# Performance work log

Hardware: AMD Instinct MI355X
Metric: run time of the kernel (lower is better)

## Reference

```python
import jax, jax.numpy as jnp
import numpy as np

N = 10000          # nodes
E = 160000         # edges (avg degree 16)
IN_DIM = 10
OUT_DIM = 3
EDGE_DIM = 9
HIDDEN = 256
HEADS = 8
C = HIDDEN // HEADS  # 32 per-head channels
T = 5
BN_EPS = 1e-5
LRELU_SLOPE = 0.2  # GATv2Conv negative_slope default


def setup_inputs() -> dict:
    key = jax.random.key(0)
    ks = jax.random.split(key, 16)
    g = lambda k, shape, scale: jax.random.normal(k, shape, dtype=jnp.float32) * scale
    s = 1.0 / np.sqrt(HIDDEN)
    inp = {}
    inp['x'] = g(ks[0], (N, IN_DIM), 1.0)
    inp['edge_attr'] = g(ks[1], (E, EDGE_DIM), 1.0)
    inp['edge_index'] = jax.random.randint(ks[2], (2, E), 0, N, dtype=jnp.int32)
    # lift
    inp['lift_W'] = g(ks[3], (IN_DIM, HIDDEN), 1.0 / np.sqrt(IN_DIM))
    inp['lift_b'] = jnp.zeros((HIDDEN,), jnp.float32)
    # T stacked GATv2 layers
    inp['Wl'] = g(ks[4], (T, HIDDEN, HIDDEN), s)
    inp['bl'] = jnp.zeros((T, HIDDEN), jnp.float32)
    inp['Wr'] = g(ks[5], (T, HIDDEN, HIDDEN), s)
    inp['br'] = jnp.zeros((T, HIDDEN), jnp.float32)
    inp['We'] = g(ks[6], (T, EDGE_DIM, HIDDEN), 1.0 / np.sqrt(EDGE_DIM))
    inp['att'] = g(ks[7], (T, HEADS, C), 1.0 / np.sqrt(C))
    inp['conv_bias'] = jnp.zeros((T, HIDDEN), jnp.float32)
    inp['bn_gamma'] = jnp.ones((T, HIDDEN), jnp.float32)
    inp['bn_beta'] = jnp.zeros((T, HIDDEN), jnp.float32)
    # projection MLP: Lin-BN-ReLU, Lin-BN-ReLU, Lin
    inp['p1_W'] = g(ks[8], (HIDDEN, HIDDEN), s)
    inp['p1_b'] = jnp.zeros((HIDDEN,), jnp.float32)
    inp['pbn1_g'] = jnp.ones((HIDDEN,), jnp.float32)
    inp['pbn1_b'] = jnp.zeros((HIDDEN,), jnp.float32)
    inp['p2_W'] = g(ks[9], (HIDDEN, HIDDEN), s)
    inp['p2_b'] = jnp.zeros((HIDDEN,), jnp.float32)
    inp['pbn2_g'] = jnp.ones((HIDDEN,), jnp.float32)
    inp['pbn2_b'] = jnp.zeros((HIDDEN,), jnp.float32)
    inp['p3_W'] = g(ks[10], (HIDDEN, OUT_DIM), s)
    inp['p3_b'] = jnp.zeros((OUT_DIM,), jnp.float32)
    return inp


def _bn(h, gamma, beta):
    # BatchNorm1d with batch statistics (biased variance), eps=1e-5
    mu = h.mean(axis=0)
    var = jnp.var(h, axis=0)
    return gamma * (h - mu) * jax.lax.rsqrt(var + BN_EPS) + beta


def _forward(x, edge_attr, edge_index, lift_W, lift_b, Wl, bl, Wr, br, We, att,
             conv_bias, bn_gamma, bn_beta, p1_W, p1_b, pbn1_g, pbn1_b,
             p2_W, p2_b, pbn2_g, pbn2_b, p3_W, p3_b):
    src = edge_index[0]  # message source j
    dst = edge_index[1]  # message target i (softmax segments)
    # per_graph_edge_norm on cols 0:9 (== full edge_dim), single graph (batch=None):
    # per-column z-score over all edges of the graph
    ea = (edge_attr - edge_attr.mean(axis=0)) / (edge_attr.std(axis=0) + 1e-8)
    h = jax.nn.relu(x @ lift_W + lift_b)  # [N, HIDDEN]
    for t in range(T):
        xl = (h @ Wl[t] + bl[t]).reshape(N, HEADS, C)   # source transform
        xr = (h @ Wr[t] + br[t]).reshape(N, HEADS, C)   # target transform
        xe = (ea @ We[t]).reshape(E, HEADS, C)          # edge transform
        # GATv2: attention logits from leaky-relu'd summed features
        e = jax.nn.leaky_relu(xl[src] + xr[dst] + xe, LRELU_SLOPE)  # [E,H,C]
        logits = jnp.einsum('ehc,hc->eh', e, att[t])                # [E,H]
        # segment softmax over destination nodes
        m = jax.ops.segment_max(logits, dst, num_segments=N)
        m = jnp.where(jnp.isfinite(m), m, 0.0)
        z = jnp.exp(logits - m[dst])
        denom = jax.ops.segment_sum(z, dst, num_segments=N)
        alpha = z / (denom[dst] + 1e-16)                             # [E,H]
        agg = jax.ops.segment_sum(alpha[:, :, None] * xl[src], dst, num_segments=N)
        out = agg.reshape(N, HIDDEN) + conv_bias[t]
        h = jax.nn.elu(_bn(out, bn_gamma[t], bn_beta[t]))
    h = jax.nn.relu(_bn(h @ p1_W + p1_b, pbn1_g, pbn1_b))
    h = jax.nn.relu(_bn(h @ p2_W + p2_b, pbn2_g, pbn2_b))
    return h @ p3_W + p3_b  # [N, OUT_DIM]


def reference(x, edge_attr, edge_index, lift_W, lift_b, Wl, bl, Wr, br, We, att,
              conv_bias, bn_gamma, bn_beta, p1_W, p1_b, pbn1_g, pbn1_b,
              p2_W, p2_b, pbn2_g, pbn2_b, p3_W, p3_b):
    return _forward(x, edge_attr, edge_index, lift_W, lift_b, Wl, bl, Wr, br, We, att,
                    conv_bias, bn_gamma, bn_beta, p1_W, p1_b, pbn1_g, pbn1_b,
                    p2_W, p2_b, pbn2_g, pbn2_b, p3_W, p3_b)
```

## Files before the change

kernel.cpp:

```cpp
#include <hip/hip_runtime.h>

#define Nn 10000
#define Ee 160000
#define HID 256
#define EDIM 9
#define INDIM 10
#define Tt 5

typedef _Float16 f16;
typedef _Float16 f16x8 __attribute__((ext_vector_type(8)));
typedef _Float16 f16x4 __attribute__((ext_vector_type(4)));
typedef float f32x4 __attribute__((ext_vector_type(4)));

__global__ __launch_bounds__(256) void colstats_kernel(const float* __restrict__ in,
                                                       float* __restrict__ cs) {
  float s[9], s2[9];
#pragma unroll
  for (int k = 0; k < 9; ++k) { s[k] = 0.f; s2[k] = 0.f; }
  for (int i = blockIdx.x * blockDim.x + threadIdx.x; i < Ee; i += gridDim.x * blockDim.x) {
#pragma unroll
    for (int k = 0; k < 9; ++k) {
      float v = in[i * 9 + k];
      s[k] += v; s2[k] += v * v;
    }
  }
#pragma unroll
  for (int k = 0; k < 9; ++k) {
    for (int off = 1; off < 64; off <<= 1) {
      s[k] += __shfl_xor(s[k], off);
      s2[k] += __shfl_xor(s2[k], off);
    }
  }
  if ((threadIdx.x & 63) == 0) {
#pragma unroll
    for (int k = 0; k < 9; ++k) {
      atomicAdd(&cs[k], s[k]);
      atomicAdd(&cs[16 + k], s2[k]);
    }
  }
}

__global__ __launch_bounds__(256) void lift_kernel(const float* __restrict__ x,
                                                   const float* __restrict__ W,
                                                   const float* __restrict__ b,
                                                   f16* __restrict__ hq) {
  __shared__ float xs[INDIM];
  int n = blockIdx.x, ch = threadIdx.x;
  if (ch < INDIM) xs[ch] = x[n * INDIM + ch];
  __syncthreads();
  float s = b[ch];
#pragma unroll
  for (int k = 0; k < INDIM; ++k) s += xs[k] * W[k * 256 + ch];
  hq[n * 256 + ch] = (f16)fmaxf(s, 0.f);
}

__global__ __launch_bounds__(256) void degree_kernel(const int* __restrict__ dst,
                                                     int* __restrict__ deg) {
  int e = blockIdx.x * 256 + threadIdx.x;
  if (e < Ee) atomicAdd(&deg[dst[e]], 1);
}

__global__ __launch_bounds__(1024) void scan_kernel(const int* __restrict__ deg,
                                                    int* __restrict__ rowptr,
                                                    int* __restrict__ cursor) {
  __shared__ int part[1024];
  int tid = threadIdx.x;
  const int CH = (Nn + 1023) / 1024;
  int start = tid * CH;
  int s = 0;
  for (int i = 0; i < CH; ++i) { int idx = start + i; if (idx < Nn) s += deg[idx]; }
  part[tid] = s;
  __syncthreads();
  for (int off = 1; off < 1024; off <<= 1) {
    int v = part[tid];
    int w = (tid >= off) ? part[tid - off] : 0;
    __syncthreads();
    part[tid] = v + w;
    __syncthreads();
  }
  int run = part[tid] - s;
  for (int i = 0; i < CH; ++i) {
    int idx = start + i;
    if (idx < Nn) { rowptr[idx] = run; cursor[idx] = run; run += deg[idx]; }
  }
  if (tid == 0) rowptr[Nn] = Ee;
}

__global__ __launch_bounds__(256) void fill_kernel(const int* __restrict__ dst,
                                                   int* __restrict__ cursor,
                                                   int* __restrict__ perm) {
  int e = blockIdx.x * 256 + threadIdx.x;
  if (e < Ee) {
    int pos = atomicAdd(&cursor[dst[e]], 1);
    perm[pos] = e;
  }
}

__global__ __launch_bounds__(256) void eaperm_kernel(const float* __restrict__ edge_attr,
                                                     const float* __restrict__ cs,
                                                     const int* __restrict__ perm,
                                                     const int* __restrict__ srcIn,
                                                     int* __restrict__ srcp,
                                                     float* __restrict__ eap) {
  int idx = blockIdx.x * 256 + threadIdx.x;
  if (idx >= Ee) return;
  int e = perm[idx];
  srcp[idx] = srcIn[e];
  const float* a = edge_attr + e * 9;
  float o[12];
#pragma unroll
  for (int k = 0; k < 9; ++k) {
    float mu = cs[k] * (1.f / Ee);
    float var = fmaxf(cs[16 + k] * (1.f / Ee) - mu * mu, 0.f);
    o[k] = (a[k] - mu) / (sqrtf(var) + 1e-8f);
  }
  o[9] = o[10] = o[11] = 0.f;
  float4 v0 = {o[0], o[1], o[2], o[3]};
  float4 v1 = {o[4], o[5], o[6], o[7]};
  float4 v2 = {o[8], o[9], o[10], o[11]};
  *(float4*)(eap + (size_t)idx * 12 + 0) = v0;
  *(float4*)(eap + (size_t)idx * 12 + 4) = v1;
  *(float4*)(eap + (size_t)idx * 12 + 8) = v2;
}

__global__ __launch_bounds__(256) void convert_kernel(const float* __restrict__ Wl,
                                                      const float* __restrict__ Wr,
                                                      const float* __restrict__ p1,
                                                      const float* __restrict__ p2,
                                                      f16* __restrict__ wt) {
  int nrow = blockIdx.x, s = blockIdx.y, k = threadIdx.x;
  const float* srcp; int n = nrow; size_t dst;
  if (s < 5) {
    dst = (size_t)s * 131072 + (size_t)nrow * 256 + k;
    if (nrow < 256) srcp = Wl + s * 65536;
    else { srcp = Wr + s * 65536; n = nrow - 256; }
  } else {
    if (nrow >= 256) return;
    dst = 655360 + (size_t)(s - 5) * 65536 + (size_t)nrow * 256 + k;
    srcp = (s == 5) ? p1 : p2;
  }
  wt[dst] = (f16)srcp[k * 256 + n];
}

__global__ __launch_bounds__(256) void prep_bias_kernel(const float* __restrict__ bl,
                                                        const float* __restrict__ br,
                                                        float* __restrict__ bc) {
  int idx = blockIdx.x * 256 + threadIdx.x;
  if (idx >= 2560) return;
  int t = idx >> 9, c = idx & 511;
  bc[idx] = (c < 256) ? bl[t * 256 + c] : br[t * 256 + c - 256];
}

__global__ __launch_bounds__(256) void gemm16_kernel(const f16* __restrict__ A,
                                                     const f16* __restrict__ BT,
                                                     const float* __restrict__ bias,
                                                     const float* __restrict__ sums,
                                                     const float* __restrict__ gamma,
                                                     const float* __restrict__ beta,
                                                     int act,
                                                     f16* __restrict__ out,
                                                     int M, int OS) {
  __shared__ __align__(16) f16 As[64][264];
  __shared__ __align__(16) f16 Bs[64][264];
  const int tid = threadIdx.x;
  const int wave = tid >> 6, lane = tid & 63;
  const int l15 = lane & 15, quad = lane >> 4;
  const int m0 = blockIdx.y * 64, n0 = blockIdx.x * 64;
  const int wm = (wave >> 1) * 32, wn = (wave & 1) * 32;
  const int colbase = (tid & 31) * 8, rowbase = tid >> 5;
  float sA[8], tA[8];
  if (act >= 0) {
#pragma unroll
    for (int c4 = 0; c4 < 2; ++c4) {
      float4 su = *(const float4*)(sums + colbase + c4 * 4);
      float4 sq = *(const float4*)(sums + 256 + colbase + c4 * 4);
      float4 g4 = *(const float4*)(gamma + colbase + c4 * 4);
      float4 b4 = *(const float4*)(beta + colbase + c4 * 4);
      float su_[4] = {su.x, su.y, su.z, su.w};
      float sq_[4] = {sq.x, sq.y, sq.z, sq.w};
      float g_[4] = {g4.x, g4.y, g4.z, g4.w};
      float b_[4] = {b4.x, b4.y, b4.z, b4.w};
#pragma unroll
      for (int c = 0; c < 4; ++c) {
        float mu = su_[c] * (1.f / Nn);
        float var = fmaxf(sq_[c] * (1.f / Nn) - mu * mu, 0.f);
        float is = rsqrtf(var + 1e-5f) * g_[c];
        sA[c4 * 4 + c] = is;
        tA[c4 * 4 + c] = b_[c] - mu * is;
      }
    }
  }
#pragma unroll
  for (int i = 0; i < 8; ++i) {
    int row = rowbase + 8 * i;
    f16x8 av = {};
    int gm = m0 + row;
    if (gm < M) av = *(const f16x8*)(A + (size_t)gm * 256 + colbase);
    if (act >= 0) {
#pragma unroll
      for (int e = 0; e < 8; ++e) {
        float y = (float)av[e] * sA[e] + tA[e];
        if (act == 0) y = y > 0.f ? y : (__expf(y) - 1.f);
        else y = fmaxf(y, 0.f);
        av[e] = (f16)y;
      }
    }
    *(f16x8*)(&As[row][colbase]) = av;
    f16x8 bv = *(const f16x8*)(BT + (size_t)(n0 + row) * 256 + colbase);
    *(f16x8*)(&Bs[row][colbase]) = bv;
  }
  __syncthreads();
  f32x4 zero4 = {0.f, 0.f, 0.f, 0.f};
  f32x4 acc[2][2] = {{zero4, zero4}, {zero4, zero4}};
#pragma unroll
  for (int kk = 0; kk < 256; kk += 32) {
    f16x8 a0 = *(const f16x8*)(&As[wm + l15][kk + quad * 8]);
    f16x8 a1 = *(const f16x8*)(&As[wm + 16 + l15][kk + quad * 8]);
    f16x8 b0 = *(const f16x8*)(&Bs[wn + l15][kk + quad * 8]);
    f16x8 b1 = *(const f16x8*)(&Bs[wn + 16 + l15][kk + quad * 8]);
    acc[0][0] = __builtin_amdgcn_mfma_f32_16x16x32_f16(a0, b0, acc[0][0], 0, 0, 0);
    acc[0][1] = __builtin_amdgcn_mfma_f32_16x16x32_f16(a0, b1, acc[0][1], 0, 0, 0);
    acc[1][0] = __builtin_amdgcn_mfma_f32_16x16x32_f16(a1, b0, acc[1][0], 0, 0, 0);
    acc[1][1] = __builtin_amdgcn_mfma_f32_16x16x32_f16(a1, b1, acc[1][1], 0, 0, 0);
  }
  __syncthreads();
  f16* Cs = (f16*)&As[0][0];
#pragma unroll
  for (int ni = 0; ni < 2; ++ni) {
    int nl = wn + ni * 16 + l15;
    float bv = bias[n0 + nl];
#pragma unroll
    for (int mi = 0; mi < 2; ++mi)
#pragma unroll
      for (int r = 0; r < 4; ++r)
        Cs[(wm + mi * 16 + quad * 4 + r) * 72 + nl] = (f16)(acc[mi][ni][r] + bv);
  }
  __syncthreads();
  {
    int row = tid >> 2, c4 = (tid & 3) * 16;
    int gm = m0 + row;
    if (gm < M) {
      f16x8 v0 = *(const f16x8*)(&Cs[row * 72 + c4]);
      f16x8 v1 = *(const f16x8*)(&Cs[row * 72 + c4 + 8]);
      *(f16x8*)(out + (size_t)gm * OS + n0 + c4) = v0;
      *(f16x8*)(out + (size_t)gm * OS + n0 + c4 + 8) = v1;
    }
  }
}

__global__ __launch_bounds__(256) void gat_fused(const f16* __restrict__ hxlr,
                                                 const float* __restrict__ eap,
                                                 const int* __restrict__ srcp,
                                                 const int* __restrict__ rowptr,
                                                 const float* __restrict__ We_t,
                                                 const float* __restrict__ att_t,
                                                 const float* __restrict__ cb_t,
                                                 f16* __restrict__ outb) {
  int wave = threadIdx.x >> 6, lane = threadIdx.x & 63;
  int i = blockIdx.x * 4 + wave;
  if (i >= Nn) return;
  int ch = lane * 4;
  float we[9][4];
#pragma unroll
  for (int k = 0; k < 9; ++k) {
    float4 w4 = *(const float4*)(We_t + k * 256 + ch);
    we[k][0] = w4.x; we[k][1] = w4.y; we[k][2] = w4.z; we[k][3] = w4.w;
  }
  float4 a4 = *(const float4*)(att_t + ch);
  float att[4] = {a4.x, a4.y, a4.z, a4.w};
  f16x4 xr4 = *(const f16x4*)(hxlr + (size_t)i * 512 + 256 + ch);
  float xri[4] = {(float)xr4[0], (float)xr4[1], (float)xr4[2], (float)xr4[3]};
  float acc[4] = {0.f, 0.f, 0.f, 0.f};
  float d = 0.f;
  int r0 = rowptr[i], r1 = rowptr[i + 1];
  for (int base = r0; base < r1; base += 4) {
    int cnt = r1 - base;
    int ib[4];
#pragma unroll
    for (int b = 0; b < 4; ++b) ib[b] = base + (b < cnt ? b : cnt - 1);
    int js[4];
#pragma unroll
    for (int b = 0; b < 4; ++b) js[b] = srcp[ib[b]];
    float xlv[4][4];
#pragma unroll
    for (int b = 0; b < 4; ++b) {
      f16x4 v4 = *(const f16x4*)(hxlr + (size_t)js[b] * 512 + ch);
      xlv[b][0] = (float)v4[0]; xlv[b][1] = (float)v4[1];
      xlv[b][2] = (float)v4[2]; xlv[b][3] = (float)v4[3];
    }
    float sp[4];
#pragma unroll
    for (int b = 0; b < 4; ++b) {
      const float* ep = eap + (size_t)ib[b] * 12;
      float4 e0 = *(const float4*)ep;
      float4 e1 = *(const float4*)(ep + 4);
      float e8 = ep[8];
      float s = 0.f;
#pragma unroll
      for (int c = 0; c < 4; ++c) {
        float v = xlv[b][c] + xri[c];
        v += e0.x * we[0][c] + e0.y * we[1][c] + e0.z * we[2][c] + e0.w * we[3][c];
        v += e1.x * we[4][c] + e1.y * we[5][c] + e1.z * we[6][c] + e1.w * we[7][c];
        v += e8 * we[8][c];
        v = v > 0.f ? v : 0.2f * v;
        s += att[c] * v;
      }
      sp[b] = s;
    }
#pragma unroll
    for (int b = 0; b < 4; ++b) {
      sp[b] += __shfl_xor(sp[b], 1);
      sp[b] += __shfl_xor(sp[b], 2);
      sp[b] += __shfl_xor(sp[b], 4);
    }
#pragma unroll
    for (int b = 0; b < 4; ++b) {
      float z = (b < cnt) ? __expf(fminf(sp[b], 75.f)) : 0.f;
      d += z;
#pragma unroll
      for (int c = 0; c < 4; ++c) acc[c] += z * xlv[b][c];
    }
  }
  float inv = 1.f / (d + 1e-16f);
  float4 cb4 = *(const float4*)(cb_t + ch);
  f16x4 o;
  o[0] = (f16)(acc[0] * inv + cb4.x);
  o[1] = (f16)(acc[1] * inv + cb4.y);
  o[2] = (f16)(acc[2] * inv + cb4.z);
  o[3] = (f16)(acc[3] * inv + cb4.w);
  *(f16x4*)(outb + (size_t)i * 256 + ch) = o;
}

__global__ __launch_bounds__(256) void bn_stats_kernel(const f16* __restrict__ v,
                                                       float* __restrict__ sums) {
  __shared__ float ls[512];
  int tid = threadIdx.x;
  for (int i = tid; i < 512; i += 256) ls[i] = 0.f;
  __syncthreads();
  int wave = tid >> 6, lane = tid & 63, ch = lane * 4;
  float s[4] = {0.f, 0.f, 0.f, 0.f}, s2[4] = {0.f, 0.f, 0.f, 0.f};
  for (int r = blockIdx.x * 4 + wave; r < Nn; r += gridDim.x * 4) {
    f16x4 x4 = *(const f16x4*)(v + (size_t)r * 256 + ch);
#pragma unroll
    for (int c = 0; c < 4; ++c) {
      float x = (float)x4[c];
      s[c] += x; s2[c] += x * x;
    }
  }
#pragma unroll
  for (int c = 0; c < 4; ++c) {
    atomicAdd(&ls[ch + c], s[c]);
    atomicAdd(&ls[256 + ch + c], s2[c]);
  }
  __syncthreads();
  for (int i = tid; i < 512; i += 256) atomicAdd(&sums[i], ls[i]);
}

__global__ __launch_bounds__(256) void final_kernel(const f16* __restrict__ hq,
                                                    const float* __restrict__ sums,
                                                    const float* __restrict__ gamma,
                                                    const float* __restrict__ beta,
                                                    const float* __restrict__ W,
                                                    const float* __restrict__ b,
                                                    float* __restrict__ out3) {
  int wave = threadIdx.x >> 6, lane = threadIdx.x & 63;
  int n = blockIdx.x * 4 + wave;
  if (n >= Nn) return;
  int ch = lane * 4;
  float4 su = *(const float4*)(sums + ch);
  float4 sq = *(const float4*)(sums + 256 + ch);
  float4 g4 = *(const float4*)(gamma + ch);
  float4 b4 = *(const float4*)(beta + ch);
  float su_[4] = {su.x, su.y, su.z, su.w};
  float sq_[4] = {sq.x, sq.y, sq.z, sq.w};
  float g_[4] = {g4.x, g4.y, g4.z, g4.w};
  float bb_[4] = {b4.x, b4.y, b4.z, b4.w};
  f16x4 h4 = *(const f16x4*)(hq + (size_t)n * 256 + ch);
  float s0 = 0.f, s1 = 0.f, s2 = 0.f;
#pragma unroll
  for (int c = 0; c < 4; ++c) {
    float mu = su_[c] * (1.f / Nn);
    float var = fmaxf(sq_[c] * (1.f / Nn) - mu * mu, 0.f);
    float is = rsqrtf(var + 1e-5f) * g_[c];
    float y = fmaxf(((float)h4[c] - mu) * is + bb_[c], 0.f);
    const float* w = W + (ch + c) * 3;
    s0 += y * w[0]; s1 += y * w[1]; s2 += y * w[2];
  }
  for (int off = 1; off < 64; off <<= 1) {
    s0 += __shfl_xor(s0, off);
    s1 += __shfl_xor(s1, off);
    s2 += __shfl_xor(s2, off);
  }
  if (lane == 0) {
    out3[n * 3 + 0] = s0 + b[0];
    out3[n * 3 + 1] = s1 + b[1];
    out3[n * 3 + 2] = s2 + b[2];
  }
}

extern "C" void kernel_launch(void* const* d_in, const int* in_sizes, int n_in,
                              void* d_out, int out_size, void* d_ws, size_t ws_size,
                              hipStream_t stream) {
  const float* x         = (const float*)d_in[0];
  const float* edge_attr = (const float*)d_in[1];
  const int*   eidx      = (const int*)d_in[2];
  const float* lift_W    = (const float*)d_in[3];
  const float* lift_b    = (const float*)d_in[4];
  const float* Wl        = (const float*)d_in[5];
  const float* bl        = (const float*)d_in[6];
  const float* Wr        = (const float*)d_in[7];
  const float* br        = (const float*)d_in[8];
  const float* We        = (const float*)d_in[9];
  const float* att       = (const float*)d_in[10];
  const float* conv_b    = (const float*)d_in[11];
  const float* bn_g      = (const float*)d_in[12];
  const float* bn_b      = (const float*)d_in[13];
  const float* p1_W      = (const float*)d_in[14];
  const float* p1_b      = (const float*)d_in[15];
  const float* pbn1_g    = (const float*)d_in[16];
  const float* pbn1_b    = (const float*)d_in[17];
  const float* p2_W      = (const float*)d_in[18];
  const float* p2_b      = (const float*)d_in[19];
  const float* pbn2_g    = (const float*)d_in[20];
  const float* pbn2_b    = (const float*)d_in[21];
  const float* p3_W      = (const float*)d_in[22];
  const float* p3_b      = (const float*)d_in[23];
  const int* srcI = eidx;
  const int* dstI = eidx + Ee;

  char* wp = (char*)d_ws;
  auto carve = [&](size_t bytes) -> void* {
    void* p = (void*)wp;
    wp += (bytes + 255) & ~(size_t)255;
    return p;
  };
  float* eap    = (float*)carve((size_t)Ee * 12 * sizeof(float));
  f16*   h16    = (f16*)carve((size_t)Nn * 256 * sizeof(f16));
  f16*   w16t   = (f16*)carve((size_t)786432 * sizeof(f16));
  float* biascat= (float*)carve((size_t)2560 * sizeof(float));
  f16*   hxlr   = (f16*)carve((size_t)Nn * 512 * sizeof(f16));
  f16*   outb16 = (f16*)carve((size_t)Nn * 256 * sizeof(f16));
  int*   deg    = (int*)carve((size_t)Nn * sizeof(int));
  int*   rowptr = (int*)carve((size_t)(Nn + 1) * sizeof(int));
  int*   cursor = (int*)carve((size_t)Nn * sizeof(int));
  int*   perm   = (int*)carve((size_t)Ee * sizeof(int));
  int*   srcp   = (int*)carve((size_t)Ee * sizeof(int));
  float* cstats = (float*)carve(32 * sizeof(float));
  float* bnsA   = (float*)carve((size_t)7 * 512 * sizeof(float));

  hipMemsetAsync(cstats, 0, 32 * sizeof(float), stream);
  hipMemsetAsync(deg, 0, Nn * sizeof(int), stream);
  hipMemsetAsync(bnsA, 0, (size_t)7 * 512 * sizeof(float), stream);

  colstats_kernel<<<64, 256, 0, stream>>>(edge_attr, cstats);
  lift_kernel<<<Nn, 256, 0, stream>>>(x, lift_W, lift_b, h16);
  degree_kernel<<<(Ee + 255) / 256, 256, 0, stream>>>(dstI, deg);
  scan_kernel<<<1, 1024, 0, stream>>>(deg, rowptr, cursor);
  fill_kernel<<<(Ee + 255) / 256, 256, 0, stream>>>(dstI, cursor, perm);
  eaperm_kernel<<<(Ee + 255) / 256, 256, 0, stream>>>(edge_attr, cstats, perm, srcI, srcp, eap);
  convert_kernel<<<dim3(512, 7), 256, 0, stream>>>(Wl, Wr, p1_W, p2_W, w16t);
  prep_bias_kernel<<<10, 256, 0, stream>>>(bl, br, biascat);

  const int MB = (Nn + 63) / 64;
  for (int t = 0; t < Tt; ++t) {
    const f16* Ain = (t == 0) ? h16 : outb16;
    const float* sums = (t == 0) ? nullptr : bnsA + (size_t)(t - 1) * 512;
    int act = (t == 0) ? -1 : 0;
    gemm16_kernel<<<dim3(8, MB), 256, 0, stream>>>(Ain, w16t + (size_t)t * 131072,
                                                   biascat + t * 512, sums,
                                                   bn_g + (t > 0 ? (t - 1) * 256 : 0),
                                                   bn_b + (t > 0 ? (t - 1) * 256 : 0),
                                                   act, hxlr, Nn, 512);
    gat_fused<<<2500, 256, 0, stream>>>(hxlr, eap, srcp, rowptr,
                                        We + t * 9 * 256, att + t * 256,
                                        conv_b + t * 256, outb16);
    bn_stats_kernel<<<128, 256, 0, stream>>>(outb16, bnsA + (size_t)t * 512);
  }
  f16* pA = hxlr;
  f16* pB = hxlr + (size_t)Nn * 256;
  gemm16_kernel<<<dim3(4, MB), 256, 0, stream>>>(outb16, w16t + 655360, p1_b,
                                                 bnsA + 4 * 512, bn_g + 4 * 256, bn_b + 4 * 256,
                                                 0, pA, Nn, 256);
  bn_stats_kernel<<<128, 256, 0, stream>>>(pA, bnsA + 5 * 512);
  gemm16_kernel<<<dim3(4, MB), 256, 0, stream>>>(pA, w16t + 720896, p2_b,
                                                 bnsA + 5 * 512, pbn1_g, pbn1_b,
                                                 1, pB, Nn, 256);
  bn_stats_kernel<<<128, 256, 0, stream>>>(pB, bnsA + 6 * 512);
  final_kernel<<<2500, 256, 0, stream>>>(pB, bnsA + 6 * 512, pbn2_g, pbn2_b, p3_W, p3_b,
                                         (float*)d_out);
}
```

Before: 623.0 us.

## Fuse BN statistics into GAT kernel with 8-way partitioned atomic sums

The batch-norm sum and sum-of-squares reduction now runs inside the GAT aggregation kernel through a shared-memory block reduce, which removes five separate bn_stats passes over the layer output. Global atomics are spread across 8 partial-sum slots indexed by block id, and the consumers (GEMM prologue, final kernel) add the 8 partials back together. The three memsets are merged into one. In exchange, gat_fused issues many more global atomics (one per block, 2500 blocks) and every consumer does extra loads. The early return was dropped; this is safe because 10000 is divisible by 4, which keeps every wave active for __syncthreads.

After: 612.4 us. Within noise of the previous version (-1.7%).

```diff
diff --git a/kernel.cpp b/kernel.cpp
--- a/kernel.cpp
+++ b/kernel.cpp
@@ -172,12 +172,16 @@
   if (act >= 0) {
 #pragma unroll
     for (int c4 = 0; c4 < 2; ++c4) {
-      float4 su = *(const float4*)(sums + colbase + c4 * 4);
-      float4 sq = *(const float4*)(sums + 256 + colbase + c4 * 4);
+      float su_[4] = {0.f, 0.f, 0.f, 0.f}, sq_[4] = {0.f, 0.f, 0.f, 0.f};
+#pragma unroll
+      for (int p = 0; p < 8; ++p) {
+        float4 su = *(const float4*)(sums + p * 512 + colbase + c4 * 4);
+        float4 sq = *(const float4*)(sums + p * 512 + 256 + colbase + c4 * 4);
+        su_[0] += su.x; su_[1] += su.y; su_[2] += su.z; su_[3] += su.w;
+        sq_[0] += sq.x; sq_[1] += sq.y; sq_[2] += sq.z; sq_[3] += sq.w;
+      }
       float4 g4 = *(const float4*)(gamma + colbase + c4 * 4);
       float4 b4 = *(const float4*)(beta + colbase + c4 * 4);
-      float su_[4] = {su.x, su.y, su.z, su.w};
-      float sq_[4] = {sq.x, sq.y, sq.z, sq.w};
       float g_[4] = {g4.x, g4.y, g4.z, g4.w};
       float b_[4] = {b4.x, b4.y, b4.z, b4.w};
 #pragma unroll
@@ -255,10 +259,11 @@
                                                  const float* __restrict__ We_t,
                                                  const float* __restrict__ att_t,
                                                  const float* __restrict__ cb_t,
-                                                 f16* __restrict__ outb) {
+                                                 f16* __restrict__ outb,
+                                                 float* __restrict__ bns) {
+  __shared__ float ls[2048];
   int wave = threadIdx.x >> 6, lane = threadIdx.x & 63;
   int i = blockIdx.x * 4 + wave;
-  if (i >= Nn) return;
   int ch = lane * 4;
   float we[9][4];
 #pragma unroll
@@ -329,6 +334,18 @@
   o[2] = (f16)(acc[2] * inv + cb4.z);
   o[3] = (f16)(acc[3] * inv + cb4.w);
   *(f16x4*)(outb + (size_t)i * 256 + ch) = o;
+#pragma unroll
+  for (int c = 0; c < 4; ++c) {
+    float xv = (float)o[c];
+    ls[wave * 512 + ch + c] = xv;
+    ls[wave * 512 + 256 + ch + c] = xv * xv;
+  }
+  __syncthreads();
+  float* bp = bns + (blockIdx.x & 7) * 512;
+  for (int q = threadIdx.x; q < 512; q += 256) {
+    float sv = ls[q] + ls[512 + q] + ls[1024 + q] + ls[1536 + q];
+    atomicAdd(&bp[q], sv);
+  }
 }
 
 __global__ __launch_bounds__(256) void bn_stats_kernel(const f16* __restrict__ v,
@@ -353,7 +370,8 @@
     atomicAdd(&ls[256 + ch + c], s2[c]);
   }
   __syncthreads();
-  for (int i = tid; i < 512; i += 256) atomicAdd(&sums[i], ls[i]);
+  float* sp2 = sums + (blockIdx.x & 7) * 512;
+  for (int i = tid; i < 512; i += 256) atomicAdd(&sp2[i], ls[i]);
 }
 
 __global__ __launch_bounds__(256) void final_kernel(const f16* __restrict__ hq,
@@ -367,12 +385,16 @@
   int n = blockIdx.x * 4 + wave;
   if (n >= Nn) return;
   int ch = lane * 4;
-  float4 su = *(const float4*)(sums + ch);
-  float4 sq = *(const float4*)(sums + 256 + ch);
+  float su_[4] = {0.f, 0.f, 0.f, 0.f}, sq_[4] = {0.f, 0.f, 0.f, 0.f};
+#pragma unroll
+  for (int p = 0; p < 8; ++p) {
+    float4 su = *(const float4*)(sums + p * 512 + ch);
+    float4 sq = *(const float4*)(sums + p * 512 + 256 + ch);
+    su_[0] += su.x; su_[1] += su.y; su_[2] += su.z; su_[3] += su.w;
+    sq_[0] += sq.x; sq_[1] += sq.y; sq_[2] += sq.z; sq_[3] += sq.w;
+  }
   float4 g4 = *(const float4*)(gamma + ch);
   float4 b4 = *(const float4*)(beta + ch);
-  float su_[4] = {su.x, su.y, su.z, su.w};
-  float sq_[4] = {sq.x, sq.y, sq.z, sq.w};
   float g_[4] = {g4.x, g4.y, g4.z, g4.w};
   float bb_[4] = {b4.x, b4.y, b4.z, b4.w};
   f16x4 h4 = *(const f16x4*)(hq + (size_t)n * 256 + ch);
@@ -434,23 +456,22 @@
     wp += (bytes + 255) & ~(size_t)255;
     return p;
   };
+  char*  zr     = (char*)carve((size_t)(32 + 7 * 4096 + Nn) * 4);
+  float* cstats = (float*)zr;
+  float* bnsA   = (float*)(zr + 32 * 4);
+  int*   deg    = (int*)(zr + (32 + 7 * 4096) * 4);
   float* eap    = (float*)carve((size_t)Ee * 12 * sizeof(float));
   f16*   h16    = (f16*)carve((size_t)Nn * 256 * sizeof(f16));
   f16*   w16t   = (f16*)carve((size_t)786432 * sizeof(f16));
   float* biascat= (float*)carve((size_t)2560 * sizeof(float));
   f16*   hxlr   = (f16*)carve((size_t)Nn * 512 * sizeof(f16));
   f16*   outb16 = (f16*)carve((size_t)Nn * 256 * sizeof(f16));
-  int*   deg    = (int*)carve((size_t)Nn * sizeof(int));
   int*   rowptr = (int*)carve((size_t)(Nn + 1) * sizeof(int));
   int*   cursor = (int*)carve((size_t)Nn * sizeof(int));
   int*   perm   = (int*)carve((size_t)Ee * sizeof(int));
   int*   srcp   = (int*)carve((size_t)Ee * sizeof(int));
-  float* cstats = (float*)carve(32 * sizeof(float));
-  float* bnsA   = (float*)carve((size_t)7 * 512 * sizeof(float));
-
-  hipMemsetAsync(cstats, 0, 32 * sizeof(float), stream);
-  hipMemsetAsync(deg, 0, Nn * sizeof(int), stream);
-  hipMemsetAsync(bnsA, 0, (size_t)7 * 512 * sizeof(float), stream);
+
+  hipMemsetAsync(zr, 0, (size_t)(32 + 7 * 4096 + Nn) * 4, stream);
 
   colstats_kernel<<<64, 256, 0, stream>>>(edge_attr, cstats);
   lift_kernel<<<Nn, 256, 0, stream>>>(x, lift_W, lift_b, h16);
@@ -464,7 +485,7 @@
   const int MB = (Nn + 63) / 64;
   for (int t = 0; t < Tt; ++t) {
     const f16* Ain = (t == 0) ? h16 : outb16;
-    const float* sums = (t == 0) ? nullptr : bnsA + (size_t)(t - 1) * 512;
+    const float* sums = (t == 0) ? nullptr : bnsA + (size_t)(t - 1) * 4096;
     int act = (t == 0) ? -1 : 0;
     gemm16_kernel<<<dim3(8, MB), 256, 0, stream>>>(Ain, w16t + (size_t)t * 131072,
                                                    biascat + t * 512, sums,
@@ -473,19 +494,19 @@
                                                    act, hxlr, Nn, 512);
     gat_fused<<<2500, 256, 0, stream>>>(hxlr, eap, srcp, rowptr,
                                         We + t * 9 * 256, att + t * 256,
-                                        conv_b + t * 256, outb16);
-    bn_stats_kernel<<<128, 256, 0, stream>>>(outb16, bnsA + (size_t)t * 512);
+                                        conv_b + t * 256, outb16,
+                                        bnsA + (size_t)t * 4096);
   }
   f16* pA = hxlr;
   f16* pB = hxlr + (size_t)Nn * 256;
   gemm16_kernel<<<dim3(4, MB), 256, 0, stream>>>(outb16, w16t + 655360, p1_b,
-                                                 bnsA + 4 * 512, bn_g + 4 * 256, bn_b + 4 * 256,
+                                                 bnsA + 4 * 4096, bn_g + 4 * 256, bn_b + 4 * 256,
                                                  0, pA, Nn, 256);
-  bn_stats_kernel<<<128, 256, 0, stream>>>(pA, bnsA + 5 * 512);
+  bn_stats_kernel<<<128, 256, 0, stream>>>(pA, bnsA + 5 * 4096);
   gemm16_kernel<<<dim3(4, MB), 256, 0, stream>>>(pA, w16t + 720896, p2_b,
-                                                 bnsA + 5 * 512, pbn1_g, pbn1_b,
+                                                 bnsA + 5 * 4096, pbn1_g, pbn1_b,
                                                  1, pB, Nn, 256);
-  bn_stats_kernel<<<128, 256, 0, stream>>>(pB, bnsA + 6 * 512);
-  final_kernel<<<2500, 256, 0, stream>>>(pB, bnsA + 6 * 512, pbn2_g, pbn2_b, p3_W, p3_b,
+  bn_stats_kernel<<<128, 256, 0, stream>>>(pB, bnsA + 6 * 4096);
+  final_kernel<<<2500, 256, 0, stream>>>(pB, bnsA + 6 * 4096, pbn2_g, pbn2_b, p3_W, p3_b,
                                          (float*)d_out);
 }
```
